# Kernel tuning notes

Hardware: AMD Instinct MI355X
Metric: run time of the kernel (lower is better)

The kernel has to match this reference:

```python
import jax, jax.numpy as jnp
import numpy as np

B, T, D = 4, 2048, 2048
H = 16
KD = D // 2          # key_dim = expand_k * d_model
VD = D               # value_dim = expand_v * d_model
DK = KD // H         # head_k_dim = 64
DV = VD // H         # head_v_dim = 128
LR = 16              # gate_low_rank_dim
EPS = 1e-5
GATE_LOGIT_NORMALIZER = 16.0


def setup_inputs() -> dict:
    key = jax.random.key(0)
    ks = jax.random.split(key, 9)
    def w(k, shape):
        fan_in = shape[0]
        return (jax.random.normal(k, shape, jnp.float32) * (fan_in ** -0.5)).astype(jnp.float32)
    return {
        "x":      jax.random.normal(ks[0], (B, T, D), jnp.float32),
        "Wq":     w(ks[1], (D, KD)),
        "Wk":     w(ks[2], (D, KD)),
        "Wv":     w(ks[3], (D, VD)),
        "Wg":     w(ks[4], (D, VD)),      # output gate projection
        "Wgk1":   w(ks[5], (D, LR)),      # gk low-rank down-proj (no bias)
        "Wgk2":   w(ks[6], (LR, KD)),     # gk up-proj
        "bgk2":   jnp.zeros((KD,), jnp.float32),
        "norm_w": jnp.ones((DV,), jnp.float32),  # per-head RMSNorm weight
        "Wo":     w(ks[7], (VD, D)),
    }


def reference(x, Wq, Wk, Wv, Wg, Wgk1, Wgk2, bgk2, norm_w, Wo):
    b, t, _ = x.shape
    dv = norm_w.shape[0]
    vd = Wv.shape[1]
    h = vd // dv
    dk = Wq.shape[1] // h
    scale = dk ** -0.5

    q = (x @ Wq).reshape(b, t, h, dk) * scale
    k = (x @ Wk).reshape(b, t, h, dk)
    v = (x @ Wv).reshape(b, t, h, dv)
    # forget gate: logsigmoid(low_rank_proj(x)) / gate_logit_normalizer
    gk = jax.nn.log_sigmoid((x @ Wgk1) @ Wgk2 + bgk2) / GATE_LOGIT_NORMALIZER
    gk = gk.reshape(b, t, h, dk)

    # time-major for scan: [T, B, H, d]
    qT = jnp.moveaxis(q, 1, 0)
    kT = jnp.moveaxis(k, 1, 0)
    vT = jnp.moveaxis(v, 1, 0)
    gT = jnp.moveaxis(gk, 1, 0)

    def step(S, inp):
        qt, kt, vt, gt = inp
        # S_t = diag(exp(gk_t)) S_{t-1} + k_t^T v_t ; shape [B,H,DK,DV]
        S = S * jnp.exp(gt)[..., None] + kt[..., None] * vt[..., None, :]
        ot = jnp.einsum('bhk,bhkv->bhv', qt, S)
        return S, ot

    S0 = jnp.zeros((b, h, dk, dv), x.dtype)
    _, o = jax.lax.scan(step, S0, (qT, kT, vT, gT))
    o = jnp.moveaxis(o, 0, 1)  # [B, T, H, DV]

    # FusedRMSNormSwishGate: rmsnorm(o) * weight * swish(g), per head dim
    g = (x @ Wg).reshape(b, t, h, dv)
    o = o * jax.lax.rsqrt(jnp.mean(o * o, axis=-1, keepdims=True) + EPS) * norm_w
    o = o * (g * jax.nn.sigmoid(g))
    return o.reshape(b, t, vd) @ Wo
```

## Files before the change

### kernel.cpp

```cpp
#include <hip/hip_runtime.h>
#include <hip/hip_bf16.h>
#include <type_traits>


using bf16x8 = __attribute__((ext_vector_type(8))) short;
using f32x4  = __attribute__((ext_vector_type(4))) float;
using f32x16 = __attribute__((ext_vector_type(16))) float;

static __device__ __forceinline__ float bf2f(ushort u) {
  union { unsigned int i; float f; } v;
  v.i = ((unsigned int)u) << 16;
  return v.f;
}
static __device__ __forceinline__ ushort f2bf(float f) {
  __hip_bfloat16 h = __float2bfloat16(f);
  return *reinterpret_cast<ushort*>(&h);
}
static __device__ __forceinline__ unsigned int pack2(float lo, float hi) {
  return (unsigned int)f2bf(lo) | ((unsigned int)f2bf(hi) << 16);
}
static __device__ __forceinline__ void unpack8(uint4 v, float* f) {
  f[0] = bf2f((ushort)(v.x & 0xffff)); f[1] = bf2f((ushort)(v.x >> 16));
  f[2] = bf2f((ushort)(v.y & 0xffff)); f[3] = bf2f((ushort)(v.y >> 16));
  f[4] = bf2f((ushort)(v.z & 0xffff)); f[5] = bf2f((ushort)(v.z >> 16));
  f[6] = bf2f((ushort)(v.w & 0xffff)); f[7] = bf2f((ushort)(v.w >> 16));
}

#define GLDS16(g, l) __builtin_amdgcn_global_load_lds( \
    (const __attribute__((address_space(1))) unsigned int*)(g), \
    (__attribute__((address_space(3))) unsigned int*)(l), 16, 0, 0)

#define SWZ3(row) ((((row) & 1) << 2) | (((row) >> 1) & 3))

__global__ __launch_bounds__(256) void f32_to_bf16(
    const float* __restrict__ in, ushort* __restrict__ out, long n) {
  long i = ((long)blockIdx.x * 256 + threadIdx.x) * 8;
  if (i >= n) return;
  float4 a = *(const float4*)(in + i);
  float4 b = *(const float4*)(in + i + 4);
  uint4 o;
  o.x = pack2(a.x, a.y); o.y = pack2(a.z, a.w);
  o.z = pack2(b.x, b.y); o.w = pack2(b.z, b.w);
  *(uint4*)(out + i) = o;
}

__global__ __launch_bounds__(256) void transpose_f32_bf16(
    const float* __restrict__ in, ushort* __restrict__ out, int R, int C) {
  __shared__ float tile[64][65];
  const int t = threadIdx.x;
  const int tc = blockIdx.x * 64;
  const int tr = blockIdx.y * 64;
  const int lr = t >> 2;
  const int lc = (t & 3) * 16;
  const float* ip = in + (long)(tr + lr) * C + tc + lc;
#pragma unroll
  for (int j = 0; j < 4; ++j)
    *(float4*)(&tile[lr][lc + j * 4]) = *(const float4*)(ip + j * 4);
  __syncthreads();
  const int c = t >> 2;
  const int r0 = (t & 3) * 16;
  ushort tmp[16];
#pragma unroll
  for (int j = 0; j < 16; ++j) tmp[j] = f2bf(tile[r0 + j][c]);
  ushort* op = out + (long)(tc + c) * R + tr + r0;
  *(uint4*)(op)     = *(uint4*)(tmp);
  *(uint4*)(op + 8) = *(uint4*)(tmp + 8);
}

template <typename OT>
__global__ __launch_bounds__(512, 2) void gemm_bt8(
    const ushort* __restrict__ A, const ushort* __restrict__ BT,
    OT* __restrict__ C, int M, int N, int K) {
  __shared__ ushort sA[2 * 16384];
  __shared__ ushort sB[2 * 16384];
  const int t = threadIdx.x;
  const int nbx = N >> 8;
  const int cpx = gridDim.x >> 3;
  const int wg = ((int)blockIdx.x & 7) * cpx + ((int)blockIdx.x >> 3);
  const int brow = (wg / nbx) * 256;
  const int bcol = (wg % nbx) * 256;

  const int w = t >> 6, l = t & 63;
  const int wm = w >> 2, wn = w & 3;
  const int l31 = l & 31, l5 = l >> 5;
  const int NT = K >> 6;

  const int srow = t >> 3;
  const int cswz = ((t & 7) ^ SWZ3(srow)) * 8;
  const ushort* Abase = A + (size_t)(brow + srow) * K + cswz;
  const ushort* Bbase = BT + (size_t)(bcol + srow) * K + cswz;
  const int t8 = t * 8;

  auto stageA = [&](int bb, int hh, int jt) {
    const ushort* s = Abase + (size_t)(hh * 128) * K + jt * 64;
    ushort* d = sA + bb * 16384 + hh * 8192 + t8;
    GLDS16(s, d);
    GLDS16(s + (size_t)64 * K, d + 4096);
  };
  auto stageB = [&](int bb, int hh, int jt) {
    const ushort* s = Bbase + (size_t)(hh * 128) * K + jt * 64;
    ushort* d = sB + bb * 16384 + hh * 8192 + t8;
    GLDS16(s, d);
    GLDS16(s + (size_t)64 * K, d + 4096);
  };

  const int swz = SWZ3(l31 & 7);
  const int aRow = (wm * 32 + l31) * 64;
  const int bRow = (wn * 32 + l31) * 64;
#define KSL(ks) ((((ks) * 2 + l5) ^ swz) * 8)

  f32x16 acc[4][2];
#pragma unroll
  for (int m = 0; m < 4; ++m)
#pragma unroll
    for (int n = 0; n < 2; ++n)
#pragma unroll
      for (int r = 0; r < 16; ++r) acc[m][n][r] = 0.f;

  stageA(0, 0, 0); stageB(0, 0, 0); stageB(0, 1, 0); stageA(0, 1, 0);
  asm volatile("s_waitcnt vmcnt(4)" ::: "memory");
  stageA(1, 0, 1); stageB(1, 0, 1); stageB(1, 1, 1);
  asm volatile("s_waitcnt vmcnt(6)" ::: "memory");
  __builtin_amdgcn_s_barrier();

  for (int kt = 0; kt < NT; ++kt) {
    const int bb = kt & 1;
    const int aOff = bb * 16384, bOff = bb * 16384;
    bf16x8 aF[2][4], bF[2][4];

#pragma unroll
    for (int mf = 0; mf < 2; ++mf)
#pragma unroll
      for (int ks = 0; ks < 4; ++ks)
        aF[mf][ks] = *(const bf16x8*)(sA + aOff + mf * 4096 + aRow + KSL(ks));
#pragma unroll
    for (int ks = 0; ks < 4; ++ks)
      bF[0][ks] = *(const bf16x8*)(sB + bOff + bRow + KSL(ks));
    if (kt + 1 < NT) stageA(bb ^ 1, 1, kt + 1);
    __builtin_amdgcn_s_barrier();
    __builtin_amdgcn_s_setprio(1);
#pragma unroll
    for (int mf = 0; mf < 2; ++mf)
#pragma unroll
      for (int ks = 0; ks < 4; ++ks)
        acc[mf][0] = __builtin_amdgcn_mfma_f32_32x32x16_bf16(aF[mf][ks], bF[0][ks], acc[mf][0], 0, 0, 0);
    __builtin_amdgcn_s_setprio(0);
    __builtin_amdgcn_s_barrier();

#pragma unroll
    for (int ks = 0; ks < 4; ++ks)
      bF[1][ks] = *(const bf16x8*)(sB + bOff + 8192 + bRow + KSL(ks));
    if (kt + 2 < NT) stageA(bb, 0, kt + 2);
    __builtin_amdgcn_s_barrier();
    __builtin_amdgcn_s_setprio(1);
#pragma unroll
    for (int mf = 0; mf < 2; ++mf)
#pragma unroll
      for (int ks = 0; ks < 4; ++ks)
        acc[mf][1] = __builtin_amdgcn_mfma_f32_32x32x16_bf16(aF[mf][ks], bF[1][ks], acc[mf][1], 0, 0, 0);
    __builtin_amdgcn_s_setprio(0);
    __builtin_amdgcn_s_barrier();

#pragma unroll
    for (int mf = 0; mf < 2; ++mf)
#pragma unroll
      for (int ks = 0; ks < 4; ++ks)
        aF[mf][ks] = *(const bf16x8*)(sA + aOff + 8192 + mf * 4096 + aRow + KSL(ks));
    if (kt + 2 < NT) stageB(bb, 0, kt + 2);
    __builtin_amdgcn_s_barrier();
    __builtin_amdgcn_s_setprio(1);
#pragma unroll
    for (int mf = 0; mf < 2; ++mf)
#pragma unroll
      for (int ks = 0; ks < 4; ++ks)
        acc[2 + mf][0] = __builtin_amdgcn_mfma_f32_32x32x16_bf16(aF[mf][ks], bF[0][ks], acc[2 + mf][0], 0, 0, 0);
    __builtin_amdgcn_s_setprio(0);
    __builtin_amdgcn_s_barrier();

    if (kt + 2 < NT) stageB(bb, 1, kt + 2);
    __builtin_amdgcn_s_barrier();
    __builtin_amdgcn_s_setprio(1);
#pragma unroll
    for (int mf = 0; mf < 2; ++mf)
#pragma unroll
      for (int ks = 0; ks < 4; ++ks)
        acc[2 + mf][1] = __builtin_amdgcn_mfma_f32_32x32x16_bf16(aF[mf][ks], bF[1][ks], acc[2 + mf][1], 0, 0, 0);
    __builtin_amdgcn_s_setprio(0);
    if (kt < NT - 2)       asm volatile("s_waitcnt vmcnt(6)" ::: "memory");
    else if (kt == NT - 2) asm volatile("s_waitcnt vmcnt(0)" ::: "memory");
    __builtin_amdgcn_s_barrier();
  }
#undef KSL

#pragma unroll
  for (int mf = 0; mf < 4; ++mf)
#pragma unroll
    for (int nf = 0; nf < 2; ++nf) {
      long col = bcol + nf * 128 + wn * 32 + l31;
      long rbase = brow + mf * 64 + wm * 32 + 4 * l5;
#pragma unroll
      for (int r = 0; r < 16; ++r) {
        long row = rbase + (r & 3) + 8 * (r >> 2);
        if constexpr (std::is_same_v<OT, ushort>) C[row * N + col] = f2bf(acc[mf][nf][r]);
        else                                      C[row * N + col] = acc[mf][nf][r];
      }
    }
}

__global__ __launch_bounds__(256) void gate_kernel(
    const ushort* __restrict__ xb, const float* __restrict__ Wgk1,
    const float* __restrict__ Wgk2, const float* __restrict__ bgk2,
    ushort* __restrict__ gbuf) {
  const int m = blockIdx.x;
  const int t = threadIdx.x;
  __shared__ float sx[2048];
  __shared__ float red[256];
  __shared__ float z1[16];
  const ushort* xr = xb + (long)m * 2048;
  {
    uint4 v = *(const uint4*)(xr + t * 8);
    float f[8];
    unpack8(v, f);
#pragma unroll
    for (int j = 0; j < 8; ++j) sx[t * 8 + j] = f[j];
  }
  __syncthreads();
  const int j = t & 15, seg = t >> 4;
  float s = 0.f;
  for (int d = 0; d < 128; ++d)
    s += sx[seg * 128 + d] * Wgk1[(seg * 128 + d) * 16 + j];
  red[t] = s;
  __syncthreads();
  if (t < 16) {
    float z = 0.f;
    for (int sg = 0; sg < 16; ++sg) z += red[sg * 16 + t];
    z1[t] = z;
  }
  __syncthreads();
#pragma unroll
  for (int r = 0; r < 4; ++r) {
    int n = r * 256 + t;
    float a = bgk2[n];
#pragma unroll
    for (int l2 = 0; l2 < 16; ++l2) a += z1[l2] * Wgk2[l2 * 1024 + n];
    float ls = fminf(a, 0.f) - log1pf(__expf(-fabsf(a)));
    gbuf[(long)m * 1024 + n] = f2bf(ls * 0.0625f);
  }
}

__global__ __launch_bounds__(256) void chunk_contrib_kernel(
    const ushort* __restrict__ qkvg, const ushort* __restrict__ gbuf,
    ushort* __restrict__ STbuf, float* __restrict__ EGtot) {
  const int blk = blockIdx.x;
  const int bh = blk >> 5, c = blk & 31;
  const int b = bh >> 4, h = bh & 15;
  const long row0 = (long)b * 2048 + c * 64;
  const int th = threadIdx.x;

  __shared__ float  gc[64][65];
  __shared__ ushort khT[64][72];
  __shared__ ushort vT[128][72];

  {
    const int t = th >> 2;
    const int k0 = (th & 3) * 16;
    const ushort* gp = gbuf + (row0 + t) * 1024 + h * 64 + k0;
    uint4 a = *(const uint4*)gp;
    uint4 b4 = *(const uint4*)(gp + 8);
    float f[8];
    unpack8(a, f);
#pragma unroll
    for (int j = 0; j < 8; ++j) gc[t][k0 + j] = f[j];
    unpack8(b4, f);
#pragma unroll
    for (int j = 0; j < 8; ++j) gc[t][k0 + 8 + j] = f[j];
  }
  __syncthreads();
  if (th < 64) {
    float s = 0.f;
    for (int t = 0; t < 64; ++t) { s += gc[t][th]; gc[t][th] = s; }
  }
  __syncthreads();
  if (th < 64) EGtot[(long)blk * 64 + th] = __expf(gc[63][th]);

  {
    const int s = th & 63, kq = th >> 6;
    const ushort* kp = qkvg + (row0 + s) * 6144 + 1024 + h * 64 + kq * 16;
    uint4 a = *(const uint4*)kp;
    uint4 b4 = *(const uint4*)(kp + 8);
    float f[16];
    unpack8(a, f); unpack8(b4, f + 8);
#pragma unroll
    for (int j = 0; j < 16; ++j) {
      int k = kq * 16 + j;
      khT[k][s] = f2bf(f[j] * __expf(gc[63][k] - gc[s][k]));
    }
    const ushort* vp = qkvg + (row0 + s) * 6144 + 2048 + h * 128 + kq * 32;
#pragma unroll
    for (int u = 0; u < 4; ++u) {
      uint4 vv = *(const uint4*)(vp + u * 8);
      const ushort* pv = (const ushort*)&vv;
#pragma unroll
      for (int j = 0; j < 8; ++j) vT[kq * 32 + u * 8 + j][s] = pv[j];
    }
  }
  __syncthreads();

  const int w = th >> 6, l = th & 63;
  const int lr = l & 15, kq8 = (l >> 4) * 8;
  f32x4 acc[4][2];
#pragma unroll
  for (int m = 0; m < 4; ++m)
#pragma unroll
    for (int n = 0; n < 2; ++n) acc[m][n] = (f32x4){0.f, 0.f, 0.f, 0.f};
#pragma unroll
  for (int ks = 0; ks < 64; ks += 32) {
#pragma unroll
    for (int m = 0; m < 4; ++m) {
      bf16x8 af = *(const bf16x8*)(&khT[m * 16 + lr][ks + kq8]);
#pragma unroll
      for (int n = 0; n < 2; ++n) {
        bf16x8 bv = *(const bf16x8*)(&vT[w * 32 + n * 16 + lr][ks + kq8]);
        acc[m][n] = __builtin_amdgcn_mfma_f32_16x16x32_bf16(af, bv, acc[m][n], 0, 0, 0);
      }
    }
  }
  ushort* Cc = STbuf + (long)blk * 8192;
  const int rq = (l >> 4) * 4;
#pragma unroll
  for (int m = 0; m < 4; ++m)
#pragma unroll
    for (int n = 0; n < 2; ++n) {
      int dv = w * 32 + n * 16 + lr;
      ushort tmp[4];
#pragma unroll
      for (int r = 0; r < 4; ++r) tmp[r] = f2bf(acc[m][n][r]);
      *(uint2*)(Cc + dv * 64 + m * 16 + rq) = *(uint2*)tmp;
    }
}

__global__ __launch_bounds__(256) void chunk_scan_kernel(
    ushort* __restrict__ STbuf, const float* __restrict__ EGtot) {
  const int blk = blockIdx.x;
  const int bh = blk >> 2, qd = blk & 3;
  const int th = threadIdx.x;
  const int dv = qd * 32 + (th >> 3);
  const int k0 = (th & 7) * 8;
  ushort* base = STbuf + (long)bh * 32 * 8192 + dv * 64 + k0;
  const float* eg = EGtot + (long)bh * 32 * 64 + k0;
  float S[8];
#pragma unroll
  for (int i = 0; i < 8; ++i) S[i] = 0.f;
  uint4 cv = *(const uint4*)base;
  float4 e0 = *(const float4*)(eg);
  float4 e1 = *(const float4*)(eg + 4);
  for (int c = 0; c < 32; ++c) {
    ushort* cur = base;
    base += 8192; eg += 64;
    uint4 nv = cv; float4 n0 = e0, n1 = e1;
    if (c < 31) {
      nv = *(const uint4*)base;
      n0 = *(const float4*)(eg);
      n1 = *(const float4*)(eg + 4);
    }
    float cf[8];
    unpack8(cv, cf);
    float ee[8] = {e0.x, e0.y, e0.z, e0.w, e1.x, e1.y, e1.z, e1.w};
    ushort so[8];
#pragma unroll
    for (int i = 0; i < 8; ++i) {
      so[i] = f2bf(S[i]);
      S[i] = S[i] * ee[i] + cf[i];
    }
    *(uint4*)cur = *(uint4*)so;
    cv = nv; e0 = n0; e1 = n1;
  }
}

__global__ __launch_bounds__(256) void chunk_output_kernel(
    const ushort* __restrict__ qkvg, const ushort* __restrict__ gbuf,
    const ushort* __restrict__ STbuf, const float* __restrict__ norm_w,
    ushort* __restrict__ oo) {
  const int blk = blockIdx.x;
  const int bh = blk >> 5, c = blk & 31;
  const int b = bh >> 4, h = bh & 15;
  const long row0 = (long)b * 2048 + c * 64;
  const int th = threadIdx.x;

  __shared__ __align__(16) char pool[71936];
  float  (*gc)[65]  = (float(*)[65])(pool);
  ushort (*qg)[72]  = (ushort(*)[72])(pool + 16640);
  ushort (*kg)[72]  = (ushort(*)[72])(pool + 25856);
  ushort (*vT)[72]  = (ushort(*)[72])(pool + 35072);
  ushort (*STs)[72] = (ushort(*)[72])(pool + 53504);
  ushort (*P)[72]   = (ushort(*)[72])(pool);

  {
    const int t = th >> 2;
    const int k0 = (th & 3) * 16;
    const ushort* gp = gbuf + (row0 + t) * 1024 + h * 64 + k0;
    uint4 a = *(const uint4*)gp;
    uint4 b4 = *(const uint4*)(gp + 8);
    float f[8];
    unpack8(a, f);
#pragma unroll
    for (int j = 0; j < 8; ++j) gc[t][k0 + j] = f[j];
    unpack8(b4, f);
#pragma unroll
    for (int j = 0; j < 8; ++j) gc[t][k0 + 8 + j] = f[j];

    const ushort* qp = qkvg + (row0 + t) * 6144 + h * 64 + k0;
    *(uint4*)(&qg[t][k0])     = *(const uint4*)qp;
    *(uint4*)(&qg[t][k0 + 8]) = *(const uint4*)(qp + 8);
    const ushort* kp = qp + 1024;
    *(uint4*)(&kg[t][k0])     = *(const uint4*)kp;
    *(uint4*)(&kg[t][k0 + 8]) = *(const uint4*)(kp + 8);
  }
  {
    const int s = th & 63, kq = th >> 6;
    const ushort* vp = qkvg + (row0 + s) * 6144 + 2048 + h * 128 + kq * 32;
#pragma unroll
    for (int u = 0; u < 4; ++u) {
      uint4 vv = *(const uint4*)(vp + u * 8);
      const ushort* pv = (const ushort*)&vv;
#pragma unroll
      for (int j = 0; j < 8; ++j) vT[kq * 32 + u * 8 + j][s] = pv[j];
    }
  }
  {
    const int row = th >> 1;
    const int col0 = (th & 1) * 32;
    const ushort* sp = STbuf + (long)blk * 8192 + row * 64 + col0;
#pragma unroll
    for (int u = 0; u < 4; ++u)
      *(uint4*)(&STs[row][col0 + u * 8]) = *(const uint4*)(sp + u * 8);
  }
  __syncthreads();
  if (th < 64) {
    float s = 0.f;
    for (int t = 0; t < 64; ++t) { s += gc[t][th]; gc[t][th] = s; }
  }
  __syncthreads();
  {
    const int t = th & 63, kb = (th >> 6) * 16;
#pragma unroll
    for (int u = 0; u < 2; ++u) {
      uint4 qv = *(const uint4*)(&qg[t][kb + u * 8]);
      uint4 kv = *(const uint4*)(&kg[t][kb + u * 8]);
      float qf[8], kf[8];
      unpack8(qv, qf); unpack8(kv, kf);
      ushort qo[8], ko[8];
#pragma unroll
      for (int j = 0; j < 8; ++j) {
        float g = gc[t][kb + u * 8 + j];
        qo[j] = f2bf(qf[j] * __expf(g) * 0.125f);
        ko[j] = f2bf(kf[j] * __expf(-g));
      }
      *(uint4*)(&qg[t][kb + u * 8]) = *(uint4*)qo;
      *(uint4*)(&kg[t][kb + u * 8]) = *(uint4*)ko;
    }
  }
  __syncthreads();

  const int w = th >> 6, l = th & 63;
  const int lr = l & 15, kq8 = (l >> 4) * 8;
  const int rq = (l >> 4) * 4;

  f32x4 acc1[4];
#pragma unroll
  for (int n = 0; n < 4; ++n) acc1[n] = (f32x4){0.f, 0.f, 0.f, 0.f};
#pragma unroll
  for (int kk = 0; kk < 64; kk += 32) {
    bf16x8 af = *(const bf16x8*)(&qg[w * 16 + lr][kk + kq8]);
#pragma unroll
    for (int n = 0; n < 4; ++n) {
      bf16x8 bv = *(const bf16x8*)(&kg[n * 16 + lr][kk + kq8]);
      acc1[n] = __builtin_amdgcn_mfma_f32_16x16x32_bf16(af, bv, acc1[n], 0, 0, 0);
    }
  }
#pragma unroll
  for (int n = 0; n < 4; ++n) {
    int s = n * 16 + lr;
#pragma unroll
    for (int r = 0; r < 4; ++r) {
      int t = w * 16 + rq + r;
      P[t][s] = f2bf(s <= t ? acc1[n][r] : 0.f);
    }
  }
  __syncthreads();

  f32x4 acc2[8];
#pragma unroll
  for (int n = 0; n < 8; ++n) acc2[n] = (f32x4){0.f, 0.f, 0.f, 0.f};
#pragma unroll
  for (int ks = 0; ks < 64; ks += 32) {
    bf16x8 af = *(const bf16x8*)(&P[w * 16 + lr][ks + kq8]);
#pragma unroll
    for (int n = 0; n < 8; ++n) {
      bf16x8 bv = *(const bf16x8*)(&vT[n * 16 + lr][ks + kq8]);
      acc2[n] = __builtin_amdgcn_mfma_f32_16x16x32_bf16(af, bv, acc2[n], 0, 0, 0);
    }
  }
#pragma unroll
  for (int kk = 0; kk < 64; kk += 32) {
    bf16x8 af = *(const bf16x8*)(&qg[w * 16 + lr][kk + kq8]);
#pragma unroll
    for (int n = 0; n < 8; ++n) {
      bf16x8 bv = *(const bf16x8*)(&STs[n * 16 + lr][kk + kq8]);
      acc2[n] = __builtin_amdgcn_mfma_f32_16x16x32_bf16(af, bv, acc2[n], 0, 0, 0);
    }
  }

  float gv[8][4];
#pragma unroll
  for (int n = 0; n < 8; ++n) {
    int dv = n * 16 + lr;
#pragma unroll
    for (int r = 0; r < 4; ++r)
      gv[n][r] = bf2f(qkvg[(row0 + w * 16 + rq + r) * 6144 + 4096 + h * 128 + dv]);
  }

  float sumsq[4] = {0.f, 0.f, 0.f, 0.f};
#pragma unroll
  for (int n = 0; n < 8; ++n)
#pragma unroll
    for (int r = 0; r < 4; ++r) sumsq[r] += acc2[n][r] * acc2[n][r];
#pragma unroll
  for (int d = 1; d < 16; d <<= 1)
#pragma unroll
    for (int r = 0; r < 4; ++r) sumsq[r] += __shfl_xor(sumsq[r], d);
  float inv[4];
#pragma unroll
  for (int r = 0; r < 4; ++r) inv[r] = rsqrtf(sumsq[r] * (1.f / 128.f) + 1e-5f);

#pragma unroll
  for (int n = 0; n < 8; ++n) {
    int dv = n * 16 + lr;
    float nw = norm_w[dv];
#pragma unroll
    for (int r = 0; r < 4; ++r) {
      float g = gv[n][r];
      float sw = g / (1.f + __expf(-g));
      oo[(row0 + w * 16 + rq + r) * 2048 + h * 128 + dv] =
          f2bf(acc2[n][r] * inv[r] * nw * sw);
    }
  }
}

extern "C" void kernel_launch(void* const* d_in, const int* in_sizes, int n_in,
                              void* d_out, int out_size, void* d_ws, size_t ws_size,
                              hipStream_t stream) {
  const float* x      = (const float*)d_in[0];
  const float* Wq     = (const float*)d_in[1];
  const float* Wk     = (const float*)d_in[2];
  const float* Wv     = (const float*)d_in[3];
  const float* Wg     = (const float*)d_in[4];
  const float* Wgk1   = (const float*)d_in[5];
  const float* Wgk2   = (const float*)d_in[6];
  const float* bgk2   = (const float*)d_in[7];
  const float* norm_w = (const float*)d_in[8];
  const float* Wo     = (const float*)d_in[9];
  float* out = (float*)d_out;

  char* ws = (char*)d_ws;
  ushort* WT    = (ushort*)(ws);
  ushort* WoT   = (ushort*)(ws + 25165824);
  ushort* qkvg  = (ushort*)(ws + 33554432);
  ushort* gbuf  = (ushort*)(ws + 134217728);
  ushort* STbuf = (ushort*)(ws + 150994944);
  ushort* xb    = (ushort*)(ws + 150994944);
  float*  EGtot = (float*)(ws + 184549376);
  ushort* oo    = (ushort*)(ws + 185073664);

  dim3 blk(256);
  f32_to_bf16<<<dim3(8192), blk, 0, stream>>>(x, xb, (long)8192 * 2048);
  transpose_f32_bf16<<<dim3(16, 32), blk, 0, stream>>>(Wq, WT, 2048, 1024);
  transpose_f32_bf16<<<dim3(16, 32), blk, 0, stream>>>(Wk, WT + (size_t)1024 * 2048, 2048, 1024);
  transpose_f32_bf16<<<dim3(32, 32), blk, 0, stream>>>(Wv, WT + (size_t)2048 * 2048, 2048, 2048);
  transpose_f32_bf16<<<dim3(32, 32), blk, 0, stream>>>(Wg, WT + (size_t)4096 * 2048, 2048, 2048);
  transpose_f32_bf16<<<dim3(32, 32), blk, 0, stream>>>(Wo, WoT, 2048, 2048);

  gemm_bt8<ushort><<<dim3(768), dim3(512), 0, stream>>>(xb, WT, qkvg, 8192, 6144, 2048);
  gate_kernel<<<dim3(8192), blk, 0, stream>>>(xb, Wgk1, Wgk2, bgk2, gbuf);

  chunk_contrib_kernel<<<dim3(2048), blk, 0, stream>>>(qkvg, gbuf, STbuf, EGtot);
  chunk_scan_kernel<<<dim3(256), blk, 0, stream>>>(STbuf, EGtot);
  chunk_output_kernel<<<dim3(2048), blk, 0, stream>>>(qkvg, gbuf, STbuf, norm_w, oo);

  gemm_bt8<float><<<dim3(256), dim3(512), 0, stream>>>(oo, WoT, out, 8192, 2048, 2048);
}
```

Baseline: 476.2 us.

## Simplify GEMM pipeline barriers and batch gate kernel over eight rows

The GEMM main loop now loads both B halves at the start of each k-step and merges the four barrier-separated compute phases into two. It issues all prefetch stages for step kt+2 after a single mid-iteration barrier, which removes several barriers per k-step. The gate kernel now processes eight rows per block, so each Wgk1/Wgk2 weight load is reused across eight tokens, and the grid shrinks to 1024 blocks. The risks are a larger live register set for the GEMM B fragments and a possible loss of overlap between global prefetches and MFMA work. The gate kernel's 64KB of shared memory may also limit occupancy.

```diff
diff --git a/kernel.cpp b/kernel.cpp
--- a/kernel.cpp
+++ b/kernel.cpp
@@ -118,41 +118,32 @@
       for (int r = 0; r < 16; ++r) acc[m][n][r] = 0.f;
 
   stageA(0, 0, 0); stageB(0, 0, 0); stageB(0, 1, 0); stageA(0, 1, 0);
-  asm volatile("s_waitcnt vmcnt(4)" ::: "memory");
   stageA(1, 0, 1); stageB(1, 0, 1); stageB(1, 1, 1);
   asm volatile("s_waitcnt vmcnt(6)" ::: "memory");
   __builtin_amdgcn_s_barrier();
 
   for (int kt = 0; kt < NT; ++kt) {
     const int bb = kt & 1;
-    const int aOff = bb * 16384, bOff = bb * 16384;
+    const int off = bb * 16384;
     bf16x8 aF[2][4], bF[2][4];
 
+    if (kt + 1 < NT) stageA(bb ^ 1, 1, kt + 1);
 #pragma unroll
     for (int mf = 0; mf < 2; ++mf)
 #pragma unroll
       for (int ks = 0; ks < 4; ++ks)
-        aF[mf][ks] = *(const bf16x8*)(sA + aOff + mf * 4096 + aRow + KSL(ks));
-#pragma unroll
-    for (int ks = 0; ks < 4; ++ks)
-      bF[0][ks] = *(const bf16x8*)(sB + bOff + bRow + KSL(ks));
-    if (kt + 1 < NT) stageA(bb ^ 1, 1, kt + 1);
-    __builtin_amdgcn_s_barrier();
+        aF[mf][ks] = *(const bf16x8*)(sA + off + mf * 4096 + aRow + KSL(ks));
+#pragma unroll
+    for (int nh = 0; nh < 2; ++nh)
+#pragma unroll
+      for (int ks = 0; ks < 4; ++ks)
+        bF[nh][ks] = *(const bf16x8*)(sB + off + nh * 8192 + bRow + KSL(ks));
     __builtin_amdgcn_s_setprio(1);
 #pragma unroll
     for (int mf = 0; mf < 2; ++mf)
 #pragma unroll
       for (int ks = 0; ks < 4; ++ks)
         acc[mf][0] = __builtin_amdgcn_mfma_f32_32x32x16_bf16(aF[mf][ks], bF[0][ks], acc[mf][0], 0, 0, 0);
-    __builtin_amdgcn_s_setprio(0);
-    __builtin_amdgcn_s_barrier();
-
-#pragma unroll
-    for (int ks = 0; ks < 4; ++ks)
-      bF[1][ks] = *(const bf16x8*)(sB + bOff + 8192 + bRow + KSL(ks));
-    if (kt + 2 < NT) stageA(bb, 0, kt + 2);
-    __builtin_amdgcn_s_barrier();
-    __builtin_amdgcn_s_setprio(1);
 #pragma unroll
     for (int mf = 0; mf < 2; ++mf)
 #pragma unroll
@@ -161,25 +152,18 @@
     __builtin_amdgcn_s_setprio(0);
     __builtin_amdgcn_s_barrier();
 
+    if (kt + 2 < NT) { stageA(bb, 0, kt + 2); stageB(bb, 0, kt + 2); stageB(bb, 1, kt + 2); }
 #pragma unroll
     for (int mf = 0; mf < 2; ++mf)
 #pragma unroll
       for (int ks = 0; ks < 4; ++ks)
-        aF[mf][ks] = *(const bf16x8*)(sA + aOff + 8192 + mf * 4096 + aRow + KSL(ks));
-    if (kt + 2 < NT) stageB(bb, 0, kt + 2);
-    __builtin_amdgcn_s_barrier();
+        aF[mf][ks] = *(const bf16x8*)(sA + off + 8192 + mf * 4096 + aRow + KSL(ks));
     __builtin_amdgcn_s_setprio(1);
 #pragma unroll
     for (int mf = 0; mf < 2; ++mf)
 #pragma unroll
       for (int ks = 0; ks < 4; ++ks)
         acc[2 + mf][0] = __builtin_amdgcn_mfma_f32_32x32x16_bf16(aF[mf][ks], bF[0][ks], acc[2 + mf][0], 0, 0, 0);
-    __builtin_amdgcn_s_setprio(0);
-    __builtin_amdgcn_s_barrier();
-
-    if (kt + 2 < NT) stageB(bb, 1, kt + 2);
-    __builtin_amdgcn_s_barrier();
-    __builtin_amdgcn_s_setprio(1);
 #pragma unroll
     for (int mf = 0; mf < 2; ++mf)
 #pragma unroll
@@ -211,40 +195,61 @@
     const ushort* __restrict__ xb, const float* __restrict__ Wgk1,
     const float* __restrict__ Wgk2, const float* __restrict__ bgk2,
     ushort* __restrict__ gbuf) {
-  const int m = blockIdx.x;
+  const long m0 = (long)blockIdx.x * 8;
   const int t = threadIdx.x;
-  __shared__ float sx[2048];
-  __shared__ float red[256];
-  __shared__ float z1[16];
-  const ushort* xr = xb + (long)m * 2048;
-  {
-    uint4 v = *(const uint4*)(xr + t * 8);
+  __shared__ float sx[8][2048];
+  __shared__ float red[16][8][16];
+  __shared__ float z1[8][16];
+#pragma unroll
+  for (int u = 0; u < 8; ++u) {
+    int idx = (u * 256 + t) * 8;
+    int r = idx >> 11, cc = idx & 2047;
+    uint4 v = *(const uint4*)(xb + (m0 + r) * 2048 + cc);
     float f[8];
     unpack8(v, f);
-#pragma unroll
-    for (int j = 0; j < 8; ++j) sx[t * 8 + j] = f[j];
-  }
-  __syncthreads();
-  const int j = t & 15, seg = t >> 4;
-  float s = 0.f;
-  for (int d = 0; d < 128; ++d)
-    s += sx[seg * 128 + d] * Wgk1[(seg * 128 + d) * 16 + j];
-  red[t] = s;
-  __syncthreads();
-  if (t < 16) {
-    float z = 0.f;
-    for (int sg = 0; sg < 16; ++sg) z += red[sg * 16 + t];
-    z1[t] = z;
-  }
-  __syncthreads();
-#pragma unroll
-  for (int r = 0; r < 4; ++r) {
-    int n = r * 256 + t;
-    float a = bgk2[n];
-#pragma unroll
-    for (int l2 = 0; l2 < 16; ++l2) a += z1[l2] * Wgk2[l2 * 1024 + n];
-    float ls = fminf(a, 0.f) - log1pf(__expf(-fabsf(a)));
-    gbuf[(long)m * 1024 + n] = f2bf(ls * 0.0625f);
+    *(float4*)(&sx[r][cc])     = (float4){f[0], f[1], f[2], f[3]};
+    *(float4*)(&sx[r][cc + 4]) = (float4){f[4], f[5], f[6], f[7]};
+  }
+  __syncthreads();
+  const int j = t & 15, dg = t >> 4;
+  float a8[8] = {0.f, 0.f, 0.f, 0.f, 0.f, 0.f, 0.f, 0.f};
+  const float* wp = Wgk1 + (dg * 128) * 16 + j;
+  for (int dc = 0; dc < 128; dc += 4) {
+    float w0 = wp[(dc + 0) * 16], w1 = wp[(dc + 1) * 16];
+    float w2 = wp[(dc + 2) * 16], w3 = wp[(dc + 3) * 16];
+    const int dd = dg * 128 + dc;
+#pragma unroll
+    for (int r = 0; r < 8; ++r) {
+      float4 xv = *(const float4*)(&sx[r][dd]);
+      a8[r] += xv.x * w0 + xv.y * w1 + xv.z * w2 + xv.w * w3;
+    }
+  }
+#pragma unroll
+  for (int r = 0; r < 8; ++r) red[dg][r][j] = a8[r];
+  __syncthreads();
+  if (t < 128) {
+    int r = t >> 4, jj = t & 15;
+    float s = 0.f;
+#pragma unroll
+    for (int g = 0; g < 16; ++g) s += red[g][r][jj];
+    z1[r][jj] = s;
+  }
+  __syncthreads();
+#pragma unroll
+  for (int q = 0; q < 4; ++q) {
+    int n = q * 256 + t;
+    float w2v[16];
+#pragma unroll
+    for (int l2 = 0; l2 < 16; ++l2) w2v[l2] = Wgk2[l2 * 1024 + n];
+    float bb = bgk2[n];
+#pragma unroll
+    for (int r = 0; r < 8; ++r) {
+      float a = bb;
+#pragma unroll
+      for (int l2 = 0; l2 < 16; ++l2) a += z1[r][l2] * w2v[l2];
+      float ls = fminf(a, 0.f) - log1pf(__expf(-fabsf(a)));
+      gbuf[(m0 + r) * 1024 + n] = f2bf(ls * 0.0625f);
+    }
   }
 }
 
@@ -581,7 +586,7 @@
   transpose_f32_bf16<<<dim3(32, 32), blk, 0, stream>>>(Wo, WoT, 2048, 2048);
 
   gemm_bt8<ushort><<<dim3(768), dim3(512), 0, stream>>>(xb, WT, qkvg, 8192, 6144, 2048);
-  gate_kernel<<<dim3(8192), blk, 0, stream>>>(xb, Wgk1, Wgk2, bgk2, gbuf);
+  gate_kernel<<<dim3(1024), blk, 0, stream>>>(xb, Wgk1, Wgk2, bgk2, gbuf);
 
   chunk_contrib_kernel<<<dim3(2048), blk, 0, stream>>>(qkvg, gbuf, STbuf, EGtot);
   chunk_scan_kernel<<<dim3(256), blk, 0, stream>>>(STbuf, EGtot);
```

Result: no change. 485.0 us (+1.9%).
